# Kernel tuning notes

Hardware: AMD Instinct MI355X
Metric: run time of the kernel (lower is better)

The kernel has to match this reference:

```python
import jax, jax.numpy as jnp
import numpy as np

EPS = 1e-5
N_MU, N_SIGMA, R_MU, R_SIGMA = 0.5, 1.25, 0.1, 0.1
B = 65536

def _noise(key, batch, feat):
    k1, k2, k3, k4 = jax.random.split(key, 4)
    mu = jax.random.uniform(k1, (feat,), minval=-N_MU, maxval=N_MU)
    sigma = jax.random.uniform(k2, (feat,), minval=1.0, maxval=N_SIGMA)
    m = mu[None, :] + jax.random.uniform(k3, (batch, feat), minval=-R_MU, maxval=R_MU)
    s = sigma[None, :] + R_SIGMA * jax.random.normal(k4, (batch, feat))
    return s.astype(jnp.float32), m.astype(jnp.float32)

def setup_inputs() -> dict:
    key = jax.random.key(0)
    ks = jax.random.split(key, 10)
    x = jax.random.normal(ks[0], (B, 784), dtype=jnp.float32)
    # Linear params (PyTorch-style fan-in init scale)
    W1 = jax.random.normal(ks[1], (300, 784), dtype=jnp.float32) / np.sqrt(784)
    b1 = jnp.zeros((300,), jnp.float32)
    W2 = jax.random.normal(ks[2], (100, 300), dtype=jnp.float32) / np.sqrt(300)
    b2 = jnp.zeros((100,), jnp.float32)
    W3 = jax.random.normal(ks[3], (10, 100), dtype=jnp.float32) / np.sqrt(100)
    b3 = jnp.zeros((10,), jnp.float32)
    g1 = jnp.ones((300,), jnp.float32); be1 = jnp.zeros((300,), jnp.float32)
    g2 = jnp.ones((100,), jnp.float32); be2 = jnp.zeros((100,), jnp.float32)
    s1, m1 = _noise(ks[4], B, 300)
    s2, m2 = _noise(ks[5], B, 100)
    return {"x": x, "W1": W1, "b1": b1, "g1": g1, "be1": be1, "s1": s1, "m1": m1,
            "W2": W2, "b2": b2, "g2": g2, "be2": be2, "s2": s2, "m2": m2,
            "W3": W3, "b3": b3}

def _batchnorm(h, gamma, beta):
    mean = jnp.mean(h, axis=0)
    var = jnp.var(h, axis=0)  # biased, as in torch training mode
    return gamma * (h - mean) * jax.lax.rsqrt(var + EPS) + beta

def reference(x, W1, b1, g1, be1, s1, m1, W2, b2, g2, be2, s2, m2, W3, b3):
    h = x.reshape(-1, 784)
    h = jax.nn.relu(h @ W1.T + b1)          # [B,300]
    h = _batchnorm(h, g1, be1)
    h = s1 * h + m1                          # AddNoise1
    h = jax.nn.relu(h @ W2.T + b2)          # [B,100]
    h = _batchnorm(h, g2, be2)
    h = s2 * h + m2                          # AddNoise2
    return h @ W3.T + b3                     # [B,10]
```

## Files before the change

kernel.cpp:

```cpp
#include <hip/hip_runtime.h>
#include <hip/hip_bf16.h>

typedef __attribute__((ext_vector_type(8))) short short8;
typedef __attribute__((ext_vector_type(4))) float f32x4;

#define NB 65536
#define EPSV 1e-5f

#define OFF_SUM1   0u
#define OFF_SQ1    1280u
#define OFF_SUM2   2560u
#define OFF_SQ2    3072u
#define OFF_A1     4096u
#define OFF_C1     5376u
#define OFF_A2     6656u
#define OFF_C2     7168u
#define OFF_W1BF   8192u
#define OFF_W2BF   524288u
#define OFF_W3BF   602112u
#define OFF_H1     1048576u
#define OFF_H2     41943040u

__device__ __forceinline__ float b2f(unsigned short u) {
  return __uint_as_float(((unsigned int)u) << 16);
}
__device__ __forceinline__ unsigned short f2b(float f) {
  __hip_bfloat16 h = __float2bfloat16(f);
  return __builtin_bit_cast(unsigned short, h);
}

__global__ void k_prep(const float* __restrict__ W1, const float* __restrict__ W2,
                       const float* __restrict__ W3, unsigned short* __restrict__ w1bf,
                       unsigned short* __restrict__ w2bf, unsigned short* __restrict__ w3bf) {
  int i = blockIdx.x * blockDim.x + threadIdx.x;
  const int N1 = 320 * 800, N2 = 112 * 320, N3 = 16 * 112;
  if (i < N1) {
    int r = i / 800, c = i % 800;
    w1bf[i] = (r < 300 && c < 784) ? f2b(W1[r * 784 + c]) : (unsigned short)0;
  } else if (i < N1 + N2) {
    int j = i - N1; int r = j / 320, c = j % 320;
    w2bf[j] = (r < 100 && c < 300) ? f2b(W2[r * 300 + c]) : (unsigned short)0;
  } else if (i < N1 + N2 + N3) {
    int j = i - N1 - N2; int r = j / 112, c = j % 112;
    w3bf[j] = (r < 10 && c < 100) ? f2b(W3[r * 100 + c]) : (unsigned short)0;
  }
}

__global__ void k_finalize(const float* __restrict__ sum, const float* __restrict__ sq,
                           const float* __restrict__ g, const float* __restrict__ be,
                           float* __restrict__ a, float* __restrict__ c, int F, int Fpad) {
  int f = blockIdx.x * blockDim.x + threadIdx.x;
  if (f >= Fpad) return;
  if (f < F) {
    float mean = sum[f] * (1.f / 65536.f);
    float var  = sq[f]  * (1.f / 65536.f) - mean * mean;
    float av   = g[f] * rsqrtf(var + EPSV);
    a[f] = av;
    c[f] = be[f] - mean * av;
  } else { a[f] = 0.f; c[f] = 0.f; }
}

__global__ __launch_bounds__(512, 2) void k_gemm1(
    const float* __restrict__ x, const float* __restrict__ b1,
    const unsigned short* __restrict__ w1bf,
    unsigned short* __restrict__ h1,
    float* __restrict__ sum1, float* __restrict__ sq1) {
  const int lane = threadIdx.x & 63, wid = threadIdx.x >> 6;
  const int wm = wid >> 2, wn = wid & 3;
  const int r = lane & 15, g = lane >> 4;
  const long rowbase = (long)blockIdx.x * 128 + wm * 64;

  f32x4 acc[4][5] = {};

  const float* xp = x + (rowbase + r) * 784 + g * 8;
  const unsigned short* bp = w1bf + (long)(wn * 80 + r) * 800 + g * 8;

  for (int k0 = 0; k0 < 784; k0 += 32) {
    short8 af[4];
    if ((k0 + g * 8) < 784) {
#pragma unroll
      for (int mt = 0; mt < 4; ++mt) {
        const float* p = xp + (long)mt * 16 * 784 + k0;
        float4 f0 = *reinterpret_cast<const float4*>(p);
        float4 f1 = *reinterpret_cast<const float4*>(p + 4);
        short8 a;
        a[0] = f2b(f0.x); a[1] = f2b(f0.y); a[2] = f2b(f0.z); a[3] = f2b(f0.w);
        a[4] = f2b(f1.x); a[5] = f2b(f1.y); a[6] = f2b(f1.z); a[7] = f2b(f1.w);
        af[mt] = a;
      }
    } else {
#pragma unroll
      for (int mt = 0; mt < 4; ++mt) af[mt] = (short8)(short)0;
    }
    short8 bfr[5];
#pragma unroll
    for (int nt = 0; nt < 5; ++nt)
      bfr[nt] = *reinterpret_cast<const short8*>(bp + (long)nt * 16 * 800 + k0);
#pragma unroll
    for (int mt = 0; mt < 4; ++mt)
#pragma unroll
      for (int nt = 0; nt < 5; ++nt)
        acc[mt][nt] = __builtin_amdgcn_mfma_f32_16x16x32_bf16(af[mt], bfr[nt], acc[mt][nt], 0, 0, 0);
  }

#pragma unroll
  for (int nt = 0; nt < 5; ++nt) {
    int col = wn * 80 + nt * 16 + r;
    float bias = (col < 300) ? b1[col] : 0.f;
    float ps = 0.f, pq = 0.f;
#pragma unroll
    for (int mt = 0; mt < 4; ++mt) {
#pragma unroll
      for (int v = 0; v < 4; ++v) {
        float val = fmaxf(acc[mt][nt][v] + bias, 0.f);
        long row = rowbase + mt * 16 + g * 4 + v;
        if (col < 304) h1[row * 304 + col] = f2b(val);
        ps += val; pq += val * val;
      }
    }
    float ts = ps + __shfl_xor(ps, 16, 64); ts += __shfl_xor(ts, 32, 64);
    float tq = pq + __shfl_xor(pq, 16, 64); tq += __shfl_xor(tq, 32, 64);
    if (g == 0) { atomicAdd(&sum1[col], ts); atomicAdd(&sq1[col], tq); }
  }
}

__global__ __launch_bounds__(512, 2) void k_gemm2(
    const unsigned short* __restrict__ h1, const float* __restrict__ s1,
    const float* __restrict__ m1, const float* __restrict__ a1,
    const float* __restrict__ c1, const float* __restrict__ b2,
    const unsigned short* __restrict__ w2bf,
    unsigned short* __restrict__ h2,
    float* __restrict__ sum2, float* __restrict__ sq2) {
  const int lane = threadIdx.x & 63, wid = threadIdx.x >> 6;
  const int r = lane & 15, g = lane >> 4;
  const long rowb = (long)blockIdx.x * 128 + wid * 16;
  const long row = rowb + r;

  f32x4 acc[7] = {};
  const unsigned short* hp = h1 + row * 304 + g * 8;
  const float* sp = s1 + row * 300 + g * 8;
  const float* mp = m1 + row * 300 + g * 8;
  const unsigned short* wp = w2bf + (long)r * 320 + g * 8;

  for (int k0 = 0; k0 < 300; k0 += 32) {
    int kb = k0 + g * 8;
    short8 af = (short8)(short)0;
    if (kb + 8 <= 300) {
      short8 h8 = *reinterpret_cast<const short8*>(hp + k0);
      float4 sA = *reinterpret_cast<const float4*>(sp + k0);
      float4 sB = *reinterpret_cast<const float4*>(sp + k0 + 4);
      float4 mA = *reinterpret_cast<const float4*>(mp + k0);
      float4 mB = *reinterpret_cast<const float4*>(mp + k0 + 4);
      float4 aA = *reinterpret_cast<const float4*>(a1 + kb);
      float4 aB = *reinterpret_cast<const float4*>(a1 + kb + 4);
      float4 cA = *reinterpret_cast<const float4*>(c1 + kb);
      float4 cB = *reinterpret_cast<const float4*>(c1 + kb + 4);
      af[0] = f2b((aA.x * b2f((unsigned short)h8[0]) + cA.x) * sA.x + mA.x);
      af[1] = f2b((aA.y * b2f((unsigned short)h8[1]) + cA.y) * sA.y + mA.y);
      af[2] = f2b((aA.z * b2f((unsigned short)h8[2]) + cA.z) * sA.z + mA.z);
      af[3] = f2b((aA.w * b2f((unsigned short)h8[3]) + cA.w) * sA.w + mA.w);
      af[4] = f2b((aB.x * b2f((unsigned short)h8[4]) + cB.x) * sB.x + mB.x);
      af[5] = f2b((aB.y * b2f((unsigned short)h8[5]) + cB.y) * sB.y + mB.y);
      af[6] = f2b((aB.z * b2f((unsigned short)h8[6]) + cB.z) * sB.z + mB.z);
      af[7] = f2b((aB.w * b2f((unsigned short)h8[7]) + cB.w) * sB.w + mB.w);
    } else if (kb < 300) {
      short8 h8 = *reinterpret_cast<const short8*>(hp + k0);
      float4 sA = *reinterpret_cast<const float4*>(sp + k0);
      float4 mA = *reinterpret_cast<const float4*>(mp + k0);
      float4 aA = *reinterpret_cast<const float4*>(a1 + kb);
      float4 cA = *reinterpret_cast<const float4*>(c1 + kb);
      af[0] = f2b((aA.x * b2f((unsigned short)h8[0]) + cA.x) * sA.x + mA.x);
      af[1] = f2b((aA.y * b2f((unsigned short)h8[1]) + cA.y) * sA.y + mA.y);
      af[2] = f2b((aA.z * b2f((unsigned short)h8[2]) + cA.z) * sA.z + mA.z);
      af[3] = f2b((aA.w * b2f((unsigned short)h8[3]) + cA.w) * sA.w + mA.w);
    }
    short8 bfr[7];
#pragma unroll
    for (int nt = 0; nt < 7; ++nt)
      bfr[nt] = *reinterpret_cast<const short8*>(wp + (long)nt * 16 * 320 + k0);
#pragma unroll
    for (int nt = 0; nt < 7; ++nt)
      acc[nt] = __builtin_amdgcn_mfma_f32_16x16x32_bf16(af, bfr[nt], acc[nt], 0, 0, 0);
  }

#pragma unroll
  for (int nt = 0; nt < 7; ++nt) {
    int col = nt * 16 + r;
    float bias = (col < 100) ? b2[col] : 0.f;
    float ps = 0.f, pq = 0.f;
#pragma unroll
    for (int v = 0; v < 4; ++v) {
      float val = fmaxf(acc[nt][v] + bias, 0.f);
      h2[(rowb + g * 4 + v) * 112 + col] = f2b(val);
      ps += val; pq += val * val;
    }
    float ts = ps + __shfl_xor(ps, 16, 64); ts += __shfl_xor(ts, 32, 64);
    float tq = pq + __shfl_xor(pq, 16, 64); tq += __shfl_xor(tq, 32, 64);
    if (g == 0) { atomicAdd(&sum2[col], ts); atomicAdd(&sq2[col], tq); }
  }
}

__global__ __launch_bounds__(512, 2) void k_gemm3(
    const unsigned short* __restrict__ h2, const float* __restrict__ s2,
    const float* __restrict__ m2, const float* __restrict__ a2,
    const float* __restrict__ c2, const float* __restrict__ b3,
    const unsigned short* __restrict__ w3bf,
    float* __restrict__ out) {
  const int lane = threadIdx.x & 63, wid = threadIdx.x >> 6;
  const int r = lane & 15, g = lane >> 4;
  const long rowb = (long)blockIdx.x * 128 + wid * 16;
  const long row = rowb + r;

  f32x4 acc = {};
  const unsigned short* hp = h2 + row * 112 + g * 8;
  const float* sp = s2 + row * 100 + g * 8;
  const float* mp = m2 + row * 100 + g * 8;
  const unsigned short* wp = w3bf + (long)r * 112 + g * 8;

  for (int k0 = 0; k0 < 112; k0 += 32) {
    int kb = k0 + g * 8;
    short8 af = (short8)(short)0;
    if (kb + 8 <= 100) {
      short8 h8 = *reinterpret_cast<const short8*>(hp + k0);
      float4 sA = *reinterpret_cast<const float4*>(sp + k0);
      float4 sB = *reinterpret_cast<const float4*>(sp + k0 + 4);
      float4 mA = *reinterpret_cast<const float4*>(mp + k0);
      float4 mB = *reinterpret_cast<const float4*>(mp + k0 + 4);
      float4 aA = *reinterpret_cast<const float4*>(a2 + kb);
      float4 aB = *reinterpret_cast<const float4*>(a2 + kb + 4);
      float4 cA = *reinterpret_cast<const float4*>(c2 + kb);
      float4 cB = *reinterpret_cast<const float4*>(c2 + kb + 4);
      af[0] = f2b((aA.x * b2f((unsigned short)h8[0]) + cA.x) * sA.x + mA.x);
      af[1] = f2b((aA.y * b2f((unsigned short)h8[1]) + cA.y) * sA.y + mA.y);
      af[2] = f2b((aA.z * b2f((unsigned short)h8[2]) + cA.z) * sA.z + mA.z);
      af[3] = f2b((aA.w * b2f((unsigned short)h8[3]) + cA.w) * sA.w + mA.w);
      af[4] = f2b((aB.x * b2f((unsigned short)h8[4]) + cB.x) * sB.x + mB.x);
      af[5] = f2b((aB.y * b2f((unsigned short)h8[5]) + cB.y) * sB.y + mB.y);
      af[6] = f2b((aB.z * b2f((unsigned short)h8[6]) + cB.z) * sB.z + mB.z);
      af[7] = f2b((aB.w * b2f((unsigned short)h8[7]) + cB.w) * sB.w + mB.w);
    } else if (kb < 100) {
      short8 h8 = *reinterpret_cast<const short8*>(hp + k0);
      float4 sA = *reinterpret_cast<const float4*>(sp + k0);
      float4 mA = *reinterpret_cast<const float4*>(mp + k0);
      float4 aA = *reinterpret_cast<const float4*>(a2 + kb);
      float4 cA = *reinterpret_cast<const float4*>(c2 + kb);
      af[0] = f2b((aA.x * b2f((unsigned short)h8[0]) + cA.x) * sA.x + mA.x);
      af[1] = f2b((aA.y * b2f((unsigned short)h8[1]) + cA.y) * sA.y + mA.y);
      af[2] = f2b((aA.z * b2f((unsigned short)h8[2]) + cA.z) * sA.z + mA.z);
      af[3] = f2b((aA.w * b2f((unsigned short)h8[3]) + cA.w) * sA.w + mA.w);
    }
    short8 bfr = *reinterpret_cast<const short8*>(wp + k0);
    acc = __builtin_amdgcn_mfma_f32_16x16x32_bf16(af, bfr, acc, 0, 0, 0);
  }

  if (r < 10) {
    float bias = b3[r];
#pragma unroll
    for (int v = 0; v < 4; ++v)
      out[(rowb + g * 4 + v) * 10 + r] = acc[v] + bias;
  }
}

extern "C" void kernel_launch(void* const* d_in, const int* in_sizes, int n_in,
                              void* d_out, int out_size, void* d_ws, size_t ws_size,
                              hipStream_t stream) {
  const float* x   = (const float*)d_in[0];
  const float* W1  = (const float*)d_in[1];
  const float* b1  = (const float*)d_in[2];
  const float* g1  = (const float*)d_in[3];
  const float* be1 = (const float*)d_in[4];
  const float* s1  = (const float*)d_in[5];
  const float* m1  = (const float*)d_in[6];
  const float* W2  = (const float*)d_in[7];
  const float* b2  = (const float*)d_in[8];
  const float* g2  = (const float*)d_in[9];
  const float* be2 = (const float*)d_in[10];
  const float* s2  = (const float*)d_in[11];
  const float* m2  = (const float*)d_in[12];
  const float* W3  = (const float*)d_in[13];
  const float* b3  = (const float*)d_in[14];

  char* ws = (char*)d_ws;
  float* sum1 = (float*)(ws + OFF_SUM1);
  float* sq1  = (float*)(ws + OFF_SQ1);
  float* sum2 = (float*)(ws + OFF_SUM2);
  float* sq2  = (float*)(ws + OFF_SQ2);
  float* a1   = (float*)(ws + OFF_A1);
  float* c1   = (float*)(ws + OFF_C1);
  float* a2   = (float*)(ws + OFF_A2);
  float* c2   = (float*)(ws + OFF_C2);
  unsigned short* w1bf = (unsigned short*)(ws + OFF_W1BF);
  unsigned short* w2bf = (unsigned short*)(ws + OFF_W2BF);
  unsigned short* w3bf = (unsigned short*)(ws + OFF_W3BF);
  unsigned short* h1   = (unsigned short*)(ws + OFF_H1);
  unsigned short* h2   = (unsigned short*)(ws + OFF_H2);

  hipMemsetAsync(ws, 0, 3584, stream);

  k_prep<<<574, 512, 0, stream>>>(W1, W2, W3, w1bf, w2bf, w3bf);
  k_gemm1<<<512, 512, 0, stream>>>(x, b1, w1bf, h1, sum1, sq1);
  k_finalize<<<1, 512, 0, stream>>>(sum1, sq1, g1, be1, a1, c1, 300, 320);
  k_gemm2<<<512, 512, 0, stream>>>(h1, s1, m1, a1, c1, b2, w2bf, h2, sum2, sq2);
  k_finalize<<<1, 512, 0, stream>>>(sum2, sq2, g2, be2, a2, c2, 100, 128);
  k_gemm3<<<512, 512, 0, stream>>>(h2, s2, m2, a2, c2, b3, w3bf, (float*)d_out);
}
```

Measured before the change: 651.9 us.

## Stage GEMM operands through swizzled LDS tiles with k-sliced weight layout

All three GEMM kernels now stage A and B tiles through XOR-swizzled shared memory each k-step. Weights are pre-laid out in 32-wide k-slices so they can be copied into LDS contiguously. In gemm1 the x tile is converted to bf16 once per block instead of redundantly by each wave, and the row tile shrinks to 64 with twice the blocks. Each k-step now needs two barriers and there is no double buffering, so loads are not overlapped with MFMA work.

```diff
diff --git a/kernel.cpp b/kernel.cpp
--- a/kernel.cpp
+++ b/kernel.cpp
@@ -4,7 +4,6 @@
 typedef __attribute__((ext_vector_type(8))) short short8;
 typedef __attribute__((ext_vector_type(4))) float f32x4;
 
-#define NB 65536
 #define EPSV 1e-5f
 
 #define OFF_SUM1   0u
@@ -15,9 +14,9 @@
 #define OFF_C1     5376u
 #define OFF_A2     6656u
 #define OFF_C2     7168u
-#define OFF_W1BF   8192u
-#define OFF_W2BF   524288u
-#define OFF_W3BF   602112u
+#define OFF_W1T    8192u
+#define OFF_W2T    524288u
+#define OFF_W3T    602112u
 #define OFF_H1     1048576u
 #define OFF_H2     41943040u
 
@@ -30,19 +29,24 @@
 }
 
 __global__ void k_prep(const float* __restrict__ W1, const float* __restrict__ W2,
-                       const float* __restrict__ W3, unsigned short* __restrict__ w1bf,
-                       unsigned short* __restrict__ w2bf, unsigned short* __restrict__ w3bf) {
+                       const float* __restrict__ W3, unsigned short* __restrict__ w1t,
+                       unsigned short* __restrict__ w2t, unsigned short* __restrict__ w3t) {
   int i = blockIdx.x * blockDim.x + threadIdx.x;
-  const int N1 = 320 * 800, N2 = 112 * 320, N3 = 16 * 112;
+  const int N1 = 25 * 320 * 32, N2 = 10 * 112 * 32, N3 = 4 * 16 * 32;
   if (i < N1) {
-    int r = i / 800, c = i % 800;
-    w1bf[i] = (r < 300 && c < 784) ? f2b(W1[r * 784 + c]) : (unsigned short)0;
+    int ks = i / (320 * 32), rem = i % (320 * 32), row = rem / 32, kk = rem % 32;
+    int k = ks * 32 + kk;
+    w1t[i] = (row < 300 && k < 784) ? f2b(W1[row * 784 + k]) : (unsigned short)0;
   } else if (i < N1 + N2) {
-    int j = i - N1; int r = j / 320, c = j % 320;
-    w2bf[j] = (r < 100 && c < 300) ? f2b(W2[r * 300 + c]) : (unsigned short)0;
+    int j = i - N1;
+    int ks = j / (112 * 32), rem = j % (112 * 32), row = rem / 32, kk = rem % 32;
+    int k = ks * 32 + kk;
+    w2t[j] = (row < 100 && k < 300) ? f2b(W2[row * 300 + k]) : (unsigned short)0;
   } else if (i < N1 + N2 + N3) {
-    int j = i - N1 - N2; int r = j / 112, c = j % 112;
-    w3bf[j] = (r < 10 && c < 100) ? f2b(W3[r * 100 + c]) : (unsigned short)0;
+    int j = i - N1 - N2;
+    int ks = j / (16 * 32), rem = j % (16 * 32), row = rem / 32, kk = rem % 32;
+    int k = ks * 32 + kk;
+    w3t[j] = (row < 10 && k < 100) ? f2b(W3[row * 100 + k]) : (unsigned short)0;
   }
 }
 
@@ -60,47 +64,70 @@
   } else { a[f] = 0.f; c[f] = 0.f; }
 }
 
-__global__ __launch_bounds__(512, 2) void k_gemm1(
+__device__ __forceinline__ unsigned int swz(int row, int c) {
+  return (unsigned int)(row * 64 + ((c ^ (row & 3)) << 4));
+}
+
+__global__ __launch_bounds__(512) void k_gemm1(
     const float* __restrict__ x, const float* __restrict__ b1,
-    const unsigned short* __restrict__ w1bf,
+    const unsigned short* __restrict__ w1t,
     unsigned short* __restrict__ h1,
     float* __restrict__ sum1, float* __restrict__ sq1) {
-  const int lane = threadIdx.x & 63, wid = threadIdx.x >> 6;
+  __shared__ __align__(16) unsigned char ldsA[64 * 64];
+  __shared__ __align__(16) unsigned char ldsB[320 * 64];
+  const int tid = threadIdx.x;
+  const int lane = tid & 63, wid = tid >> 6;
   const int wm = wid >> 2, wn = wid & 3;
   const int r = lane & 15, g = lane >> 4;
-  const long rowbase = (long)blockIdx.x * 128 + wm * 64;
-
-  f32x4 acc[4][5] = {};
-
-  const float* xp = x + (rowbase + r) * 784 + g * 8;
-  const unsigned short* bp = w1bf + (long)(wn * 80 + r) * 800 + g * 8;
-
-  for (int k0 = 0; k0 < 784; k0 += 32) {
-    short8 af[4];
-    if ((k0 + g * 8) < 784) {
-#pragma unroll
-      for (int mt = 0; mt < 4; ++mt) {
-        const float* p = xp + (long)mt * 16 * 784 + k0;
+  const long rowbase = (long)blockIdx.x * 64;
+
+  f32x4 acc[2][5] = {};
+
+  for (int ks = 0; ks < 25; ++ks) {
+    if (tid < 256) {
+      int row = tid >> 2, c = tid & 3;
+      int kb = ks * 32 + c * 8;
+      short8 v = (short8)(short)0;
+      if (kb + 8 <= 784) {
+        const float* p = x + (rowbase + row) * 784 + kb;
         float4 f0 = *reinterpret_cast<const float4*>(p);
         float4 f1 = *reinterpret_cast<const float4*>(p + 4);
-        short8 a;
-        a[0] = f2b(f0.x); a[1] = f2b(f0.y); a[2] = f2b(f0.z); a[3] = f2b(f0.w);
-        a[4] = f2b(f1.x); a[5] = f2b(f1.y); a[6] = f2b(f1.z); a[7] = f2b(f1.w);
-        af[mt] = a;
-      }
-    } else {
-#pragma unroll
-      for (int mt = 0; mt < 4; ++mt) af[mt] = (short8)(short)0;
-    }
-    short8 bfr[5];
-#pragma unroll
-    for (int nt = 0; nt < 5; ++nt)
-      bfr[nt] = *reinterpret_cast<const short8*>(bp + (long)nt * 16 * 800 + k0);
-#pragma unroll
-    for (int mt = 0; mt < 4; ++mt)
+        v[0] = f2b(f0.x); v[1] = f2b(f0.y); v[2] = f2b(f0.z); v[3] = f2b(f0.w);
+        v[4] = f2b(f1.x); v[5] = f2b(f1.y); v[6] = f2b(f1.z); v[7] = f2b(f1.w);
+      }
+      *reinterpret_cast<short8*>(&ldsA[swz(row, c)]) = v;
+    }
+    {
+      const unsigned short* wsrc = w1t + ks * (320 * 32);
+      int s = tid;
+#pragma unroll
+      for (int it = 0; it < 3; ++it) {
+        if (it < 2 || s < 1280) {
+          short8 v = *reinterpret_cast<const short8*>(wsrc + s * 8);
+          *reinterpret_cast<short8*>(&ldsB[swz(s >> 2, s & 3)]) = v;
+        }
+        s += 512;
+      }
+    }
+    __syncthreads();
+
+    short8 af[2], bfr[5];
+#pragma unroll
+    for (int mt = 0; mt < 2; ++mt) {
+      int row = wm * 32 + mt * 16 + r;
+      af[mt] = *reinterpret_cast<const short8*>(&ldsA[swz(row, g)]);
+    }
+#pragma unroll
+    for (int nt = 0; nt < 5; ++nt) {
+      int row = wn * 80 + nt * 16 + r;
+      bfr[nt] = *reinterpret_cast<const short8*>(&ldsB[swz(row, g)]);
+    }
+#pragma unroll
+    for (int mt = 0; mt < 2; ++mt)
 #pragma unroll
       for (int nt = 0; nt < 5; ++nt)
         acc[mt][nt] = __builtin_amdgcn_mfma_f32_16x16x32_bf16(af[mt], bfr[nt], acc[mt][nt], 0, 0, 0);
+    __syncthreads();
   }
 
 #pragma unroll
@@ -109,11 +136,11 @@
     float bias = (col < 300) ? b1[col] : 0.f;
     float ps = 0.f, pq = 0.f;
 #pragma unroll
-    for (int mt = 0; mt < 4; ++mt) {
+    for (int mt = 0; mt < 2; ++mt) {
 #pragma unroll
       for (int v = 0; v < 4; ++v) {
         float val = fmaxf(acc[mt][nt][v] + bias, 0.f);
-        long row = rowbase + mt * 16 + g * 4 + v;
+        long row = rowbase + wm * 32 + mt * 16 + g * 4 + v;
         if (col < 304) h1[row * 304 + col] = f2b(val);
         ps += val; pq += val * val;
       }
@@ -124,65 +151,77 @@
   }
 }
 
-__global__ __launch_bounds__(512, 2) void k_gemm2(
+__global__ __launch_bounds__(512) void k_gemm2(
     const unsigned short* __restrict__ h1, const float* __restrict__ s1,
     const float* __restrict__ m1, const float* __restrict__ a1,
     const float* __restrict__ c1, const float* __restrict__ b2,
-    const unsigned short* __restrict__ w2bf,
+    const unsigned short* __restrict__ w2t,
     unsigned short* __restrict__ h2,
     float* __restrict__ sum2, float* __restrict__ sq2) {
-  const int lane = threadIdx.x & 63, wid = threadIdx.x >> 6;
+  __shared__ __align__(16) unsigned char ldsA[128 * 64];
+  __shared__ __align__(16) unsigned char ldsB[112 * 64];
+  const int tid = threadIdx.x, lane = tid & 63, wid = tid >> 6;
   const int r = lane & 15, g = lane >> 4;
-  const long rowb = (long)blockIdx.x * 128 + wid * 16;
-  const long row = rowb + r;
+  const long rowbase = (long)blockIdx.x * 128;
 
   f32x4 acc[7] = {};
-  const unsigned short* hp = h1 + row * 304 + g * 8;
-  const float* sp = s1 + row * 300 + g * 8;
-  const float* mp = m1 + row * 300 + g * 8;
-  const unsigned short* wp = w2bf + (long)r * 320 + g * 8;
-
-  for (int k0 = 0; k0 < 300; k0 += 32) {
-    int kb = k0 + g * 8;
-    short8 af = (short8)(short)0;
-    if (kb + 8 <= 300) {
-      short8 h8 = *reinterpret_cast<const short8*>(hp + k0);
-      float4 sA = *reinterpret_cast<const float4*>(sp + k0);
-      float4 sB = *reinterpret_cast<const float4*>(sp + k0 + 4);
-      float4 mA = *reinterpret_cast<const float4*>(mp + k0);
-      float4 mB = *reinterpret_cast<const float4*>(mp + k0 + 4);
-      float4 aA = *reinterpret_cast<const float4*>(a1 + kb);
-      float4 aB = *reinterpret_cast<const float4*>(a1 + kb + 4);
-      float4 cA = *reinterpret_cast<const float4*>(c1 + kb);
-      float4 cB = *reinterpret_cast<const float4*>(c1 + kb + 4);
-      af[0] = f2b((aA.x * b2f((unsigned short)h8[0]) + cA.x) * sA.x + mA.x);
-      af[1] = f2b((aA.y * b2f((unsigned short)h8[1]) + cA.y) * sA.y + mA.y);
-      af[2] = f2b((aA.z * b2f((unsigned short)h8[2]) + cA.z) * sA.z + mA.z);
-      af[3] = f2b((aA.w * b2f((unsigned short)h8[3]) + cA.w) * sA.w + mA.w);
-      af[4] = f2b((aB.x * b2f((unsigned short)h8[4]) + cB.x) * sB.x + mB.x);
-      af[5] = f2b((aB.y * b2f((unsigned short)h8[5]) + cB.y) * sB.y + mB.y);
-      af[6] = f2b((aB.z * b2f((unsigned short)h8[6]) + cB.z) * sB.z + mB.z);
-      af[7] = f2b((aB.w * b2f((unsigned short)h8[7]) + cB.w) * sB.w + mB.w);
-    } else if (kb < 300) {
-      short8 h8 = *reinterpret_cast<const short8*>(hp + k0);
-      float4 sA = *reinterpret_cast<const float4*>(sp + k0);
-      float4 mA = *reinterpret_cast<const float4*>(mp + k0);
-      float4 aA = *reinterpret_cast<const float4*>(a1 + kb);
-      float4 cA = *reinterpret_cast<const float4*>(c1 + kb);
-      af[0] = f2b((aA.x * b2f((unsigned short)h8[0]) + cA.x) * sA.x + mA.x);
-      af[1] = f2b((aA.y * b2f((unsigned short)h8[1]) + cA.y) * sA.y + mA.y);
-      af[2] = f2b((aA.z * b2f((unsigned short)h8[2]) + cA.z) * sA.z + mA.z);
-      af[3] = f2b((aA.w * b2f((unsigned short)h8[3]) + cA.w) * sA.w + mA.w);
-    }
-    short8 bfr[7];
-#pragma unroll
-    for (int nt = 0; nt < 7; ++nt)
-      bfr[nt] = *reinterpret_cast<const short8*>(wp + (long)nt * 16 * 320 + k0);
-#pragma unroll
-    for (int nt = 0; nt < 7; ++nt)
-      acc[nt] = __builtin_amdgcn_mfma_f32_16x16x32_bf16(af, bfr[nt], acc[nt], 0, 0, 0);
-  }
-
+
+  for (int ks = 0; ks < 10; ++ks) {
+    {
+      int row = tid >> 2, c = tid & 3;
+      int kb = ks * 32 + c * 8;
+      long grow = rowbase + row;
+      short8 v = (short8)(short)0;
+      if (kb + 8 <= 300) {
+        short8 h8 = *reinterpret_cast<const short8*>(h1 + grow * 304 + kb);
+        float4 sA = *reinterpret_cast<const float4*>(s1 + grow * 300 + kb);
+        float4 sB = *reinterpret_cast<const float4*>(s1 + grow * 300 + kb + 4);
+        float4 mA = *reinterpret_cast<const float4*>(m1 + grow * 300 + kb);
+        float4 mB = *reinterpret_cast<const float4*>(m1 + grow * 300 + kb + 4);
+        float4 aA = *reinterpret_cast<const float4*>(a1 + kb);
+        float4 aB = *reinterpret_cast<const float4*>(a1 + kb + 4);
+        float4 cA = *reinterpret_cast<const float4*>(c1 + kb);
+        float4 cB = *reinterpret_cast<const float4*>(c1 + kb + 4);
+        v[0] = f2b(fmaf(fmaf(aA.x, b2f((unsigned short)h8[0]), cA.x), sA.x, mA.x));
+        v[1] = f2b(fmaf(fmaf(aA.y, b2f((unsigned short)h8[1]), cA.y), sA.y, mA.y));
+        v[2] = f2b(fmaf(fmaf(aA.z, b2f((unsigned short)h8[2]), cA.z), sA.z, mA.z));
+        v[3] = f2b(fmaf(fmaf(aA.w, b2f((unsigned short)h8[3]), cA.w), sA.w, mA.w));
+        v[4] = f2b(fmaf(fmaf(aB.x, b2f((unsigned short)h8[4]), cB.x), sB.x, mB.x));
+        v[5] = f2b(fmaf(fmaf(aB.y, b2f((unsigned short)h8[5]), cB.y), sB.y, mB.y));
+        v[6] = f2b(fmaf(fmaf(aB.z, b2f((unsigned short)h8[6]), cB.z), sB.z, mB.z));
+        v[7] = f2b(fmaf(fmaf(aB.w, b2f((unsigned short)h8[7]), cB.w), sB.w, mB.w));
+      } else if (kb < 300) {
+        short8 h8 = *reinterpret_cast<const short8*>(h1 + grow * 304 + kb);
+        float4 sA = *reinterpret_cast<const float4*>(s1 + grow * 300 + kb);
+        float4 mA = *reinterpret_cast<const float4*>(m1 + grow * 300 + kb);
+        float4 aA = *reinterpret_cast<const float4*>(a1 + kb);
+        float4 cA = *reinterpret_cast<const float4*>(c1 + kb);
+        v[0] = f2b(fmaf(fmaf(aA.x, b2f((unsigned short)h8[0]), cA.x), sA.x, mA.x));
+        v[1] = f2b(fmaf(fmaf(aA.y, b2f((unsigned short)h8[1]), cA.y), sA.y, mA.y));
+        v[2] = f2b(fmaf(fmaf(aA.z, b2f((unsigned short)h8[2]), cA.z), sA.z, mA.z));
+        v[3] = f2b(fmaf(fmaf(aA.w, b2f((unsigned short)h8[3]), cA.w), sA.w, mA.w));
+      }
+      *reinterpret_cast<short8*>(&ldsA[swz(row, c)]) = v;
+    }
+    if (wid < 7) {
+      int s = wid * 64 + lane;
+      short8 v = *reinterpret_cast<const short8*>(w2t + ks * (112 * 32) + s * 8);
+      *reinterpret_cast<short8*>(&ldsB[swz(s >> 2, s & 3)]) = v;
+    }
+    __syncthreads();
+
+    int arow = wid * 16 + r;
+    short8 af = *reinterpret_cast<const short8*>(&ldsA[swz(arow, g)]);
+#pragma unroll
+    for (int nt = 0; nt < 7; ++nt) {
+      int brow = nt * 16 + r;
+      short8 bfr = *reinterpret_cast<const short8*>(&ldsB[swz(brow, g)]);
+      acc[nt] = __builtin_amdgcn_mfma_f32_16x16x32_bf16(af, bfr, acc[nt], 0, 0, 0);
+    }
+    __syncthreads();
+  }
+
+  const long rowb = rowbase + wid * 16;
 #pragma unroll
   for (int nt = 0; nt < 7; ++nt) {
     int col = nt * 16 + r;
@@ -200,59 +239,72 @@
   }
 }
 
-__global__ __launch_bounds__(512, 2) void k_gemm3(
+__global__ __launch_bounds__(512) void k_gemm3(
     const unsigned short* __restrict__ h2, const float* __restrict__ s2,
     const float* __restrict__ m2, const float* __restrict__ a2,
     const float* __restrict__ c2, const float* __restrict__ b3,
-    const unsigned short* __restrict__ w3bf,
+    const unsigned short* __restrict__ w3t,
     float* __restrict__ out) {
-  const int lane = threadIdx.x & 63, wid = threadIdx.x >> 6;
+  __shared__ __align__(16) unsigned char ldsA[128 * 64];
+  __shared__ __align__(16) unsigned char ldsB[16 * 64];
+  const int tid = threadIdx.x, lane = tid & 63, wid = tid >> 6;
   const int r = lane & 15, g = lane >> 4;
-  const long rowb = (long)blockIdx.x * 128 + wid * 16;
-  const long row = rowb + r;
+  const long rowbase = (long)blockIdx.x * 128;
 
   f32x4 acc = {};
-  const unsigned short* hp = h2 + row * 112 + g * 8;
-  const float* sp = s2 + row * 100 + g * 8;
-  const float* mp = m2 + row * 100 + g * 8;
-  const unsigned short* wp = w3bf + (long)r * 112 + g * 8;
-
-  for (int k0 = 0; k0 < 112; k0 += 32) {
-    int kb = k0 + g * 8;
-    short8 af = (short8)(short)0;
-    if (kb + 8 <= 100) {
-      short8 h8 = *reinterpret_cast<const short8*>(hp + k0);
-      float4 sA = *reinterpret_cast<const float4*>(sp + k0);
-      float4 sB = *reinterpret_cast<const float4*>(sp + k0 + 4);
-      float4 mA = *reinterpret_cast<const float4*>(mp + k0);
-      float4 mB = *reinterpret_cast<const float4*>(mp + k0 + 4);
-      float4 aA = *reinterpret_cast<const float4*>(a2 + kb);
-      float4 aB = *reinterpret_cast<const float4*>(a2 + kb + 4);
-      float4 cA = *reinterpret_cast<const float4*>(c2 + kb);
-      float4 cB = *reinterpret_cast<const float4*>(c2 + kb + 4);
-      af[0] = f2b((aA.x * b2f((unsigned short)h8[0]) + cA.x) * sA.x + mA.x);
-      af[1] = f2b((aA.y * b2f((unsigned short)h8[1]) + cA.y) * sA.y + mA.y);
-      af[2] = f2b((aA.z * b2f((unsigned short)h8[2]) + cA.z) * sA.z + mA.z);
-      af[3] = f2b((aA.w * b2f((unsigned short)h8[3]) + cA.w) * sA.w + mA.w);
-      af[4] = f2b((aB.x * b2f((unsigned short)h8[4]) + cB.x) * sB.x + mB.x);
-      af[5] = f2b((aB.y * b2f((unsigned short)h8[5]) + cB.y) * sB.y + mB.y);
-      af[6] = f2b((aB.z * b2f((unsigned short)h8[6]) + cB.z) * sB.z + mB.z);
-      af[7] = f2b((aB.w * b2f((unsigned short)h8[7]) + cB.w) * sB.w + mB.w);
-    } else if (kb < 100) {
-      short8 h8 = *reinterpret_cast<const short8*>(hp + k0);
-      float4 sA = *reinterpret_cast<const float4*>(sp + k0);
-      float4 mA = *reinterpret_cast<const float4*>(mp + k0);
-      float4 aA = *reinterpret_cast<const float4*>(a2 + kb);
-      float4 cA = *reinterpret_cast<const float4*>(c2 + kb);
-      af[0] = f2b((aA.x * b2f((unsigned short)h8[0]) + cA.x) * sA.x + mA.x);
-      af[1] = f2b((aA.y * b2f((unsigned short)h8[1]) + cA.y) * sA.y + mA.y);
-      af[2] = f2b((aA.z * b2f((unsigned short)h8[2]) + cA.z) * sA.z + mA.z);
-      af[3] = f2b((aA.w * b2f((unsigned short)h8[3]) + cA.w) * sA.w + mA.w);
-    }
-    short8 bfr = *reinterpret_cast<const short8*>(wp + k0);
+
+  for (int ks = 0; ks < 4; ++ks) {
+    {
+      int row = tid >> 2, c = tid & 3;
+      int kb = ks * 32 + c * 8;
+      long grow = rowbase + row;
+      short8 v = (short8)(short)0;
+      if (kb + 8 <= 100) {
+        short8 h8 = *reinterpret_cast<const short8*>(h2 + grow * 112 + kb);
+        float4 sA = *reinterpret_cast<const float4*>(s2 + grow * 100 + kb);
+        float4 sB = *reinterpret_cast<const float4*>(s2 + grow * 100 + kb + 4);
+        float4 mA = *reinterpret_cast<const float4*>(m2 + grow * 100 + kb);
+        float4 mB = *reinterpret_cast<const float4*>(m2 + grow * 100 + kb + 4);
+        float4 aA = *reinterpret_cast<const float4*>(a2 + kb);
+        float4 aB = *reinterpret_cast<const float4*>(a2 + kb + 4);
+        float4 cA = *reinterpret_cast<const float4*>(c2 + kb);
+        float4 cB = *reinterpret_cast<const float4*>(c2 + kb + 4);
+        v[0] = f2b(fmaf(fmaf(aA.x, b2f((unsigned short)h8[0]), cA.x), sA.x, mA.x));
+        v[1] = f2b(fmaf(fmaf(aA.y, b2f((unsigned short)h8[1]), cA.y), sA.y, mA.y));
+        v[2] = f2b(fmaf(fmaf(aA.z, b2f((unsigned short)h8[2]), cA.z), sA.z, mA.z));
+        v[3] = f2b(fmaf(fmaf(aA.w, b2f((unsigned short)h8[3]), cA.w), sA.w, mA.w));
+        v[4] = f2b(fmaf(fmaf(aB.x, b2f((unsigned short)h8[4]), cB.x), sB.x, mB.x));
+        v[5] = f2b(fmaf(fmaf(aB.y, b2f((unsigned short)h8[5]), cB.y), sB.y, mB.y));
+        v[6] = f2b(fmaf(fmaf(aB.z, b2f((unsigned short)h8[6]), cB.z), sB.z, mB.z));
+        v[7] = f2b(fmaf(fmaf(aB.w, b2f((unsigned short)h8[7]), cB.w), sB.w, mB.w));
+      } else if (kb < 100) {
+        short8 h8 = *reinterpret_cast<const short8*>(h2 + grow * 112 + kb);
+        float4 sA = *reinterpret_cast<const float4*>(s2 + grow * 100 + kb);
+        float4 mA = *reinterpret_cast<const float4*>(m2 + grow * 100 + kb);
+        float4 aA = *reinterpret_cast<const float4*>(a2 + kb);
+        float4 cA = *reinterpret_cast<const float4*>(c2 + kb);
+        v[0] = f2b(fmaf(fmaf(aA.x, b2f((unsigned short)h8[0]), cA.x), sA.x, mA.x));
+        v[1] = f2b(fmaf(fmaf(aA.y, b2f((unsigned short)h8[1]), cA.y), sA.y, mA.y));
+        v[2] = f2b(fmaf(fmaf(aA.z, b2f((unsigned short)h8[2]), cA.z), sA.z, mA.z));
+        v[3] = f2b(fmaf(fmaf(aA.w, b2f((unsigned short)h8[3]), cA.w), sA.w, mA.w));
+      }
+      *reinterpret_cast<short8*>(&ldsA[swz(row, c)]) = v;
+    }
+    if (wid == 0) {
+      int s = lane;
+      short8 v = *reinterpret_cast<const short8*>(w3t + ks * (16 * 32) + s * 8);
+      *reinterpret_cast<short8*>(&ldsB[swz(s >> 2, s & 3)]) = v;
+    }
+    __syncthreads();
+
+    int arow = wid * 16 + r;
+    short8 af = *reinterpret_cast<const short8*>(&ldsA[swz(arow, g)]);
+    short8 bfr = *reinterpret_cast<const short8*>(&ldsB[swz(r, g)]);
     acc = __builtin_amdgcn_mfma_f32_16x16x32_bf16(af, bfr, acc, 0, 0, 0);
-  }
-
+    __syncthreads();
+  }
+
+  const long rowb = rowbase + wid * 16;
   if (r < 10) {
     float bias = b3[r];
 #pragma unroll
@@ -289,18 +341,18 @@
   float* c1   = (float*)(ws + OFF_C1);
   float* a2   = (float*)(ws + OFF_A2);
   float* c2   = (float*)(ws + OFF_C2);
-  unsigned short* w1bf = (unsigned short*)(ws + OFF_W1BF);
-  unsigned short* w2bf = (unsigned short*)(ws + OFF_W2BF);
-  unsigned short* w3bf = (unsigned short*)(ws + OFF_W3BF);
-  unsigned short* h1   = (unsigned short*)(ws + OFF_H1);
-  unsigned short* h2   = (unsigned short*)(ws + OFF_H2);
+  unsigned short* w1t = (unsigned short*)(ws + OFF_W1T);
+  unsigned short* w2t = (unsigned short*)(ws + OFF_W2T);
+  unsigned short* w3t = (unsigned short*)(ws + OFF_W3T);
+  unsigned short* h1  = (unsigned short*)(ws + OFF_H1);
+  unsigned short* h2  = (unsigned short*)(ws + OFF_H2);
 
   hipMemsetAsync(ws, 0, 3584, stream);
 
-  k_prep<<<574, 512, 0, stream>>>(W1, W2, W3, w1bf, w2bf, w3bf);
-  k_gemm1<<<512, 512, 0, stream>>>(x, b1, w1bf, h1, sum1, sq1);
+  k_prep<<<574, 512, 0, stream>>>(W1, W2, W3, w1t, w2t, w3t);
+  k_gemm1<<<1024, 512, 0, stream>>>(x, b1, w1t, h1, sum1, sq1);
   k_finalize<<<1, 512, 0, stream>>>(sum1, sq1, g1, be1, a1, c1, 300, 320);
-  k_gemm2<<<512, 512, 0, stream>>>(h1, s1, m1, a1, c1, b2, w2bf, h2, sum2, sq2);
+  k_gemm2<<<512, 512, 0, stream>>>(h1, s1, m1, a1, c1, b2, w2t, h2, sum2, sq2);
   k_finalize<<<1, 512, 0, stream>>>(sum2, sq2, g2, be2, a2, c2, 100, 128);
-  k_gemm3<<<512, 512, 0, stream>>>(h2, s2, m2, a2, c2, b3, w3bf, (float*)d_out);
-}
+  k_gemm3<<<512, 512, 0, stream>>>(h2, s2, m2, a2, c2, b3, w3t, (float*)d_out);
+}
```

Measured after the change: 646.2 us. Within noise of the previous version (-0.9%).
